# Kernel tuning notes

Hardware: AMD Instinct MI355X
Metric: run time of the kernel (lower is better)

The kernel has to match this reference:

```python
import jax, jax.numpy as jnp
import numpy as np

B, T, C, H = 8, 1024, 768, 12
HD = C // H  # 64, even for RoPE
ROPE_THETA = 10000.0


def precompute_freqs_cis(dim, end, theta=ROPE_THETA):
    # [end, dim//2, 2] with (cos, sin) in last axis
    freqs = 1.0 / theta ** (jnp.arange(0, dim // 2).astype(jnp.float32) / (dim // 2))
    t = jnp.arange(end)
    f = jnp.outer(t, freqs)
    return jnp.stack([jnp.cos(f), jnp.sin(f)], axis=-1)


def apply_rope(x, fc):
    # x: [B,T,H,hd]; fc: [T,1,hd//2,2] (broadcasts over B and H)
    xr = x.reshape(*x.shape[:-1], -1, 2)
    x_re, x_im = xr[..., 0], xr[..., 1]
    cos, sin = fc[..., 0], fc[..., 1]
    out_re = x_re * cos - x_im * sin
    out_im = x_re * sin + x_im * cos
    return jnp.stack([out_re, out_im], axis=-1).reshape(x.shape)


def setup_inputs() -> dict:
    key = jax.random.key(0)
    k0, k1, k2 = jax.random.split(key, 3)
    x = jax.random.normal(k0, (B, T, C), jnp.float32)
    Wqkv = jax.random.normal(k1, (C, 3 * C), jnp.float32) * 0.02
    bqkv = jnp.zeros((3 * C,), jnp.float32)
    Wproj = jax.random.normal(k2, (C, C), jnp.float32) * 0.02
    bproj = jnp.zeros((C,), jnp.float32)
    mask = jnp.tril(jnp.ones((T, T), jnp.int32))  # causal
    return {"x": x, "Wqkv": Wqkv, "bqkv": bqkv, "Wproj": Wproj, "bproj": bproj, "mask": mask}


def reference(x, Wqkv, bqkv, Wproj, bproj, mask):
    B_, T_, C_ = x.shape
    qkv = (x @ Wqkv + bqkv).reshape(B_, T_, 3, H, HD)
    q, k, v = qkv[:, :, 0], qkv[:, :, 1], qkv[:, :, 2]  # each [B,T,H,hd]
    fc = precompute_freqs_cis(HD, T_)[:, None]  # [T,1,hd//2,2]
    q = apply_rope(q, fc)
    k = apply_rope(k, fc)
    scale = 1.0 / jnp.sqrt(jnp.float32(HD))
    attn = jnp.einsum('bthd,bkhd->bhtk', q, k) * scale  # [B,H,T,T]
    neg = jnp.finfo(attn.dtype).min
    attn = jnp.where(mask[None, None, :, :] == 0, neg, attn)
    attn = jax.nn.softmax(attn, axis=-1)
    out = jnp.einsum('bhtk,bkhd->bthd', attn, v).reshape(B_, T_, C_)
    return out @ Wproj + bproj
```

## Files before the change

### kernel.cpp

```cpp
#include <hip/hip_runtime.h>
#include <cstdint>
#include <cstddef>

#define BB 8
#define TT 1024
#define CC 768
#define NH 12
#define HD 64

using bf16x8 = __attribute__((ext_vector_type(8))) short;
using f32x4  = __attribute__((ext_vector_type(4))) float;

static __device__ __forceinline__ short f2bf(float f) {
    uint32_t u;
    __builtin_memcpy(&u, &f, 4);
    u += 0x7FFFu + ((u >> 16) & 1u);
    return (short)(u >> 16);
}

static __device__ __forceinline__ uint32_t bfpack(float lo, float hi) {
    return (uint32_t)(uint16_t)f2bf(lo) | ((uint32_t)(uint16_t)f2bf(hi) << 16);
}

#define GLOAD_LDS16(gp, lp)                                                        \
    __builtin_amdgcn_global_load_lds(                                              \
        (const __attribute__((address_space(1))) void*)(gp),                       \
        (__attribute__((address_space(3))) void*)(lp), 16, 0, 0)

__global__ void fc_kernel(float2* __restrict__ fc) {
    int idx = blockIdx.x * 256 + threadIdx.x;
    int t = idx >> 5, p = idx & 31;
    float freq = powf(10000.0f, -(float)p / 32.0f);
    float a = (float)t * freq;
    fc[idx] = make_float2(cosf(a), sinf(a));
}

__global__ __launch_bounds__(256)
void cast_kernel(const float* __restrict__ in, short* __restrict__ out) {
    int i = (blockIdx.x * 256 + threadIdx.x) * 8;
    float4 f0 = *(const float4*)(in + i);
    float4 f1 = *(const float4*)(in + i + 4);
    bf16x8 h;
    h[0] = f2bf(f0.x); h[1] = f2bf(f0.y); h[2] = f2bf(f0.z); h[3] = f2bf(f0.w);
    h[4] = f2bf(f1.x); h[5] = f2bf(f1.y); h[6] = f2bf(f1.z); h[7] = f2bf(f1.w);
    *(bf16x8*)(out + i) = h;
}

__global__ __launch_bounds__(256)
void transpose_cast_kernel(const float* __restrict__ in, short* __restrict__ out,
                           int R, int Cdim) {
    __shared__ float tile[32][33];
    int tx = threadIdx.x, ty = threadIdx.y;
    int c0 = blockIdx.x * 32, r0 = blockIdx.y * 32;
#pragma unroll
    for (int i = 0; i < 4; i++)
        tile[ty + 8 * i][tx] = in[(size_t)(r0 + ty + 8 * i) * Cdim + c0 + tx];
    __syncthreads();
#pragma unroll
    for (int i = 0; i < 4; i++)
        out[(size_t)(c0 + ty + 8 * i) * R + r0 + tx] = f2bf(tile[tx][ty + 8 * i]);
}

__global__ __launch_bounds__(256)
void vtrans_kernel(const short* __restrict__ V, short* __restrict__ VT) {
    __shared__ short tl[64][72];
    const int tid = threadIdx.x;
    const int bh = blockIdx.y, t0 = blockIdx.x * 64;
    {
        int r = tid >> 2, cs = (tid & 3) * 16;
        const short* src = V + (size_t)bh * TT * HD + (size_t)(t0 + r) * HD + cs;
        *(bf16x8*)&tl[r][cs]     = *(const bf16x8*)src;
        *(bf16x8*)&tl[r][cs + 8] = *(const bf16x8*)(src + 8);
    }
    __syncthreads();
    {
        int d = tid >> 2, ts = (tid & 3) * 16;
        bf16x8 o0, o1;
#pragma unroll
        for (int e = 0; e < 8; e++) { o0[e] = tl[ts + e][d]; o1[e] = tl[ts + 8 + e][d]; }
        short* dst = VT + (size_t)bh * TT * HD + (size_t)d * TT + t0 + ts;
        *(bf16x8*)dst       = o0;
        *(bf16x8*)(dst + 8) = o1;
    }
}

template <int EPI>
__global__ __launch_bounds__(256)
void gemm_kernel(const short* __restrict__ Agl, const short* __restrict__ BT,
                 const float* __restrict__ bias,
                 short* __restrict__ Qb, short* __restrict__ Kb, short* __restrict__ Vb,
                 const float2* __restrict__ fc, float* __restrict__ out) {
    __shared__ __align__(16) char smem[49152];
    const int tid = threadIdx.x;
    const int lane = tid & 63, wid = tid >> 6;
    const int g = lane >> 4, c = lane & 15;
    const int wm = wid >> 1, wn = wid & 1;

    const int nx = gridDim.x;
    const int bid = blockIdx.y * nx + blockIdx.x;
    const int cpx = (nx * gridDim.y) >> 3;
    const int swz = (bid & 7) * cpx + (bid >> 3);
    const int m0 = (swz / nx) * 128, n0 = (swz % nx) * 128;

    const int sr = lane >> 2;
    const int scol = (((lane & 3) ^ ((sr >> 1) & 3)) << 3);
    const short* Abase = Agl + (size_t)(m0 + wid * 32 + sr) * 768 + scol;
    const short* Bbase = BT  + (size_t)(n0 + wid * 32 + sr) * 768 + scol;

#define STAGE(S, T, KH)                                                          \
    {                                                                            \
        size_t ko = (size_t)(T) * 64 + (KH) * 32;                                \
        GLOAD_LDS16(Abase + ko,            smem + (S) * 16384 + wid * 2048);     \
        GLOAD_LDS16(Abase + 16 * 768 + ko, smem + (S) * 16384 + wid * 2048 + 1024); \
        GLOAD_LDS16(Bbase + ko,            smem + (S) * 16384 + 8192 + wid * 2048); \
        GLOAD_LDS16(Bbase + 16 * 768 + ko, smem + (S) * 16384 + 8192 + wid * 2048 + 1024); \
    }

    const f32x4 zero4 = {0.f, 0.f, 0.f, 0.f};
    f32x4 acc[4][4];
#pragma unroll
    for (int i = 0; i < 4; i++)
#pragma unroll
        for (int j = 0; j < 4; j++) acc[i][j] = zero4;

    STAGE(0, 0, 0);
    STAGE(1, 0, 1);
    asm volatile("s_waitcnt vmcnt(4)" ::: "memory");
    asm volatile("s_barrier" ::: "memory");

    for (int t3 = 0; t3 < 12; t3 += 3) {
#pragma unroll
        for (int pp = 0; pp < 6; pp++) {
            const int slotR = pp % 3;
            const int slotS = (pp + 2) % 3;
            const int tile = t3 + (pp >> 1);
            const int kk = pp & 1;
            int tileS = tile + 1;
            if (tileS >= 12) tileS -= 12;

            const short* Ab = (const short*)(smem + slotR * 16384);
            const short* Bb = (const short*)(smem + slotR * 16384 + 8192);
            bf16x8 af[4], bfr[4];
#pragma unroll
            for (int mi = 0; mi < 4; mi++) {
                int row = wm * 64 + mi * 16 + c;
                af[mi] = *(const bf16x8*)&Ab[row * 32 + ((g ^ ((row >> 1) & 3)) << 3)];
            }
#pragma unroll
            for (int ni = 0; ni < 4; ni++) {
                int row = wn * 64 + ni * 16 + c;
                bfr[ni] = *(const bf16x8*)&Bb[row * 32 + ((g ^ ((row >> 1) & 3)) << 3)];
            }
            STAGE(slotS, tileS, kk);
            __builtin_amdgcn_s_setprio(1);
#pragma unroll
            for (int mi = 0; mi < 4; mi++)
#pragma unroll
                for (int ni = 0; ni < 4; ni++)
                    acc[mi][ni] = __builtin_amdgcn_mfma_f32_16x16x32_bf16(
                        af[mi], bfr[ni], acc[mi][ni], 0, 0, 0);
            __builtin_amdgcn_s_setprio(0);
            asm volatile("s_waitcnt vmcnt(4)" ::: "memory");
            asm volatile("s_barrier" ::: "memory");
        }
    }

    asm volatile("s_waitcnt vmcnt(0)" ::: "memory");
    asm volatile("s_barrier" ::: "memory");

    if (EPI == 0) {
        uint32_t* LD = (uint32_t*)smem;
#pragma unroll
        for (int ni = 0; ni < 4; ni++) {
            int nl = wn * 64 + ni * 16 + c;
            int n = n0 + nl;
            float bv = bias[n];
            int part = (n >= 1536) ? 2 : (n >= 768 ? 1 : 0);
            int d = (n - part * 768) & 63;
#pragma unroll
            for (int mi = 0; mi < 4; mi++) {
#pragma unroll
                for (int r = 0; r < 4; r++) {
                    int ml = wm * 64 + mi * 16 + g * 4 + r;
                    float v = acc[mi][ni][r] + bv;
                    float pv = __shfl_xor(v, 1);
                    if (!(c & 1)) {
                        float o0, o1;
                        if (part < 2) {
                            int t = (m0 + ml) & 1023;
                            float2 cs = fc[t * 32 + (d >> 1)];
                            o0 = v * cs.x - pv * cs.y;
                            o1 = v * cs.y + pv * cs.x;
                            if (part == 0) { o0 *= 0.125f; o1 *= 0.125f; }
                        } else { o0 = v; o1 = pv; }
                        LD[ml * 64 + ((nl >> 1) ^ (((ml >> 2) & 3) << 3))] = bfpack(o0, o1);
                    }
                }
            }
        }
        __syncthreads();
#pragma unroll
        for (int p = 0; p < 8; p++) {
            int ml = p * 16 + (tid >> 4);
            int wc = (tid & 15) * 4;
            int4 dat = *(const int4*)&LD[ml * 64 + (wc ^ (((ml >> 2) & 3) << 3))];
            int n = n0 + wc * 2;
            int part = (n >= 1536) ? 2 : (n >= 768 ? 1 : 0);
            int rem = n - part * 768;
            int h = rem >> 6, d = rem & 63;
            int m = m0 + ml, b = m >> 10, t = m & 1023;
            short* dst = (part == 0 ? Qb : part == 1 ? Kb : Vb)
                         + (((size_t)b * NH + h) * TT + t) * HD + d;
            *(int4*)dst = dat;
        }
    } else {
#pragma unroll
        for (int mi = 0; mi < 4; mi++)
#pragma unroll
            for (int ni = 0; ni < 4; ni++) {
                int n = n0 + wn * 64 + ni * 16 + c;
                float bv = bias[n];
#pragma unroll
                for (int r = 0; r < 4; r++) {
                    int m = m0 + wm * 64 + mi * 16 + g * 4 + r;
                    out[(size_t)m * CC + n] = acc[mi][ni][r] + bv;
                }
            }
    }
#undef STAGE
}

__global__ __launch_bounds__(256)
void attn_kernel(const short* __restrict__ Qb, const short* __restrict__ Kb,
                 const short* __restrict__ VT, short* __restrict__ Ob) {
    __shared__ uint32_t Pt[4][32][32];
    __shared__ uint32_t ot[128 * 32];
    const int tid = threadIdx.x, lane = tid & 63, wid = tid >> 6;
    const int g = lane >> 4, c = lane & 15;
    const int bh = blockIdx.x, qb = 7 - (int)blockIdx.y;
    const int b = bh / NH, h = bh % NH;
    const short* Qp = Qb + (size_t)bh * TT * HD;
    const short* Kp = Kb + (size_t)bh * TT * HD;
    const short* Vp = VT + (size_t)bh * TT * HD;
    const int q0 = qb * 128 + wid * 32;
    const int sw = (c & 7) << 2;

    bf16x8 qf[2][2];
#pragma unroll
    for (int qs = 0; qs < 2; qs++)
#pragma unroll
        for (int kh = 0; kh < 2; kh++)
            qf[qs][kh] = *(const bf16x8*)(Qp + (size_t)(q0 + qs * 16 + c) * HD + kh * 32 + g * 8);

    const f32x4 zero4 = {0.f, 0.f, 0.f, 0.f};
    f32x4 o[2][4];
#pragma unroll
    for (int qs = 0; qs < 2; qs++)
#pragma unroll
        for (int dt = 0; dt < 4; dt++) o[qs][dt] = zero4;
    float mrun[2] = {-1e30f, -1e30f}, lrun[2] = {0.f, 0.f};

    const int t0max = ((q0 + 31) >> 6) << 6;
    for (int t0 = 0; t0 <= t0max; t0 += 64) {
        f32x4 st[2][4];
#pragma unroll
        for (int nt = 0; nt < 4; nt++) {
            const short* kp = Kp + (size_t)(t0 + nt * 16 + c) * HD + g * 8;
            bf16x8 k0 = *(const bf16x8*)kp;
            bf16x8 k1 = *(const bf16x8*)(kp + 32);
#pragma unroll
            for (int qs = 0; qs < 2; qs++) {
                f32x4 z = zero4;
                z = __builtin_amdgcn_mfma_f32_16x16x32_bf16(k0, qf[qs][0], z, 0, 0, 0);
                z = __builtin_amdgcn_mfma_f32_16x16x32_bf16(k1, qf[qs][1], z, 0, 0, 0);
                st[qs][nt] = z;
            }
        }
        bf16x8 vf[2][4];
#pragma unroll
        for (int blk = 0; blk < 2; blk++)
#pragma unroll
            for (int dt = 0; dt < 4; dt++)
                vf[blk][dt] = *(const bf16x8*)(Vp + (size_t)(dt * 16 + c) * TT + t0 + blk * 32 + g * 8);
        if (t0 + 63 > q0) {
#pragma unroll
            for (int qs = 0; qs < 2; qs++) {
                int q = q0 + qs * 16 + c;
#pragma unroll
                for (int nt = 0; nt < 4; nt++)
#pragma unroll
                    for (int r = 0; r < 4; r++)
                        if (t0 + nt * 16 + g * 4 + r > q) st[qs][nt][r] = -1e30f;
            }
        }
#pragma unroll
        for (int qs = 0; qs < 2; qs++) {
            float mx = st[qs][0][0];
#pragma unroll
            for (int nt = 0; nt < 4; nt++)
#pragma unroll
                for (int r = 0; r < 4; r++) mx = fmaxf(mx, st[qs][nt][r]);
            mx = fmaxf(mx, __shfl_xor(mx, 16));
            mx = fmaxf(mx, __shfl_xor(mx, 32));
            float mnew = fmaxf(mrun[qs], mx);
            float al = __expf(mrun[qs] - mnew);
            mrun[qs] = mnew;
            float sm = 0.f;
#pragma unroll
            for (int nt = 0; nt < 4; nt++)
#pragma unroll
                for (int r = 0; r < 4; r++) {
                    float e = __expf(st[qs][nt][r] - mnew);
                    st[qs][nt][r] = e;
                    sm += e;
                }
            sm += __shfl_xor(sm, 16);
            sm += __shfl_xor(sm, 32);
            lrun[qs] = lrun[qs] * al + sm;
#pragma unroll
            for (int dt = 0; dt < 4; dt++) {
                o[qs][dt][0] *= al; o[qs][dt][1] *= al;
                o[qs][dt][2] *= al; o[qs][dt][3] *= al;
            }
            int row = qs * 16 + c;
#pragma unroll
            for (int nt = 0; nt < 4; nt++) {
                uint32_t w0 = bfpack(st[qs][nt][0], st[qs][nt][1]);
                uint32_t w1 = bfpack(st[qs][nt][2], st[qs][nt][3]);
                int wa = nt * 8 + 2 * g;
                Pt[wid][row][wa ^ sw]       = w0;
                Pt[wid][row][(wa + 1) ^ sw] = w1;
            }
        }
#pragma unroll
        for (int qs = 0; qs < 2; qs++) {
            int row = qs * 16 + c;
#pragma unroll
            for (int blk = 0; blk < 2; blk++) {
                bf16x8 pf = *(const bf16x8*)&Pt[wid][row][(blk * 16 + 4 * g) ^ sw];
#pragma unroll
                for (int dt = 0; dt < 4; dt++)
                    o[qs][dt] = __builtin_amdgcn_mfma_f32_16x16x32_bf16(
                        vf[blk][dt], pf, o[qs][dt], 0, 0, 0);
            }
        }
    }

#pragma unroll
    for (int qs = 0; qs < 2; qs++) {
        float inv = 1.0f / lrun[qs];
        int ql = wid * 32 + qs * 16 + c;
#pragma unroll
        for (int dt = 0; dt < 4; dt++) {
            uint32_t w0 = bfpack(o[qs][dt][0] * inv, o[qs][dt][1] * inv);
            uint32_t w1 = bfpack(o[qs][dt][2] * inv, o[qs][dt][3] * inv);
            int jc0 = dt * 8 + 2 * g;
            int jc1 = jc0 + 1;
            ot[ql * 32 + ((((jc0 >> 2) ^ (c & 7)) << 2) | (jc0 & 3))] = w0;
            ot[ql * 32 + ((((jc1 >> 2) ^ (c & 7)) << 2) | (jc1 & 3))] = w1;
        }
    }
    __syncthreads();
#pragma unroll
    for (int p = 0; p < 4; p++) {
        int q = (tid >> 3) + 32 * p;
        int jb = tid & 7;
        const uint32_t* src = &ot[q * 32 + ((jb ^ (q & 7)) << 2)];
        int4 w = *(const int4*)src;
        *(int4*)(Ob + ((size_t)b * TT + qb * 128 + q) * CC + h * HD + jb * 8) = w;
    }
}

extern "C" void kernel_launch(void* const* d_in, const int* in_sizes, int n_in,
                              void* d_out, int out_size, void* d_ws, size_t ws_size,
                              hipStream_t stream) {
    const float* x     = (const float*)d_in[0];
    const float* Wqkv  = (const float*)d_in[1];
    const float* bqkv  = (const float*)d_in[2];
    const float* Wproj = (const float*)d_in[3];
    const float* bproj = (const float*)d_in[4];

    char* ws = (char*)d_ws;
    short*  WqkvT  = (short*)(ws);
    short*  WprojT = (short*)(ws + 3538944);
    float2* fc     = (float2*)(ws + 3538944 + 1179648);
    short*  Qb     = (short*)(ws + 4980736);
    short*  Kb     = (short*)(ws + 4980736 + 1 * 12582912);
    short*  VOb    = (short*)(ws + 4980736 + 2 * 12582912);
    short*  VbT    = (short*)(ws + 4980736 + 3 * 12582912);
    short*  xb     = VbT;
    float*  out    = (float*)d_out;

    hipLaunchKernelGGL(fc_kernel, dim3(128), dim3(256), 0, stream, fc);
    hipLaunchKernelGGL(transpose_cast_kernel, dim3(72, 24), dim3(32, 8), 0, stream,
                       Wqkv, WqkvT, 768, 2304);
    hipLaunchKernelGGL(transpose_cast_kernel, dim3(24, 24), dim3(32, 8), 0, stream,
                       Wproj, WprojT, 768, 768);
    hipLaunchKernelGGL(cast_kernel, dim3(3072), dim3(256), 0, stream, x, xb);
    hipLaunchKernelGGL((gemm_kernel<0>), dim3(18, 64), dim3(256), 0, stream,
                       xb, WqkvT, bqkv, Qb, Kb, VOb, fc, (float*)nullptr);
    hipLaunchKernelGGL(vtrans_kernel, dim3(16, 96), dim3(256), 0, stream, VOb, VbT);
    hipLaunchKernelGGL(attn_kernel, dim3(96, 8), dim3(256), 0, stream, Qb, Kb, VbT, VOb);
    hipLaunchKernelGGL((gemm_kernel<1>), dim3(6, 64), dim3(256), 0, stream,
                       VOb, WprojT, bproj,
                       (short*)nullptr, (short*)nullptr, (short*)nullptr,
                       (const float2*)nullptr, out);
}
```

Before: 170.0 us.

## Enlarge GEMM tiles to 256x256 with 512 threads and four-stage LDS pipeline

Both GEMMs (QKV projection and output projection) move from 128x128 block tiles with 256 threads and a three-slot pipeline to 256x256 tiles with 512 threads (8 waves). The K loop now steps by 32 through a four-slot, 128 KB LDS ring, prefetching three tiles ahead. The QKV epilogue staging layout and its swizzle are widened to match. The aim is more operand reuse per byte loaded and fewer redundant global reads. In exchange the grids shrink to 288 and 96 blocks, which leaves CUs idle or adds tail waves on a 256-CU part, and the large LDS footprint limits occupancy.

```diff
diff --git a/kernel.cpp b/kernel.cpp
--- a/kernel.cpp
+++ b/kernel.cpp
@@ -85,82 +85,80 @@
 }
 
 template <int EPI>
-__global__ __launch_bounds__(256)
+__global__ __launch_bounds__(512, 2)
 void gemm_kernel(const short* __restrict__ Agl, const short* __restrict__ BT,
                  const float* __restrict__ bias,
                  short* __restrict__ Qb, short* __restrict__ Kb, short* __restrict__ Vb,
                  const float2* __restrict__ fc, float* __restrict__ out) {
-    __shared__ __align__(16) char smem[49152];
+    __shared__ __align__(16) char smem[131072];
     const int tid = threadIdx.x;
     const int lane = tid & 63, wid = tid >> 6;
     const int g = lane >> 4, c = lane & 15;
-    const int wm = wid >> 1, wn = wid & 1;
+    const int wm = wid >> 2, wn = wid & 3;
 
     const int nx = gridDim.x;
     const int bid = blockIdx.y * nx + blockIdx.x;
     const int cpx = (nx * gridDim.y) >> 3;
     const int swz = (bid & 7) * cpx + (bid >> 3);
-    const int m0 = (swz / nx) * 128, n0 = (swz % nx) * 128;
-
-    const int sr = lane >> 2;
-    const int scol = (((lane & 3) ^ ((sr >> 1) & 3)) << 3);
-    const short* Abase = Agl + (size_t)(m0 + wid * 32 + sr) * 768 + scol;
-    const short* Bbase = BT  + (size_t)(n0 + wid * 32 + sr) * 768 + scol;
-
-#define STAGE(S, T, KH)                                                          \
+    const int m0 = (swz / nx) * 256, n0 = (swz % nx) * 256;
+
+    const int srow = (lane >> 2);
+    const int schunk = (lane & 3) ^ ((lane >> 3) & 3);
+    const short* Ab0 = Agl + (size_t)(m0 + wid * 16 + srow) * 768 + schunk * 8;
+    const short* Bb0 = BT  + (size_t)(n0 + wid * 16 + srow) * 768 + schunk * 8;
+
+#define STAGE(S, T)                                                              \
     {                                                                            \
-        size_t ko = (size_t)(T) * 64 + (KH) * 32;                                \
-        GLOAD_LDS16(Abase + ko,            smem + (S) * 16384 + wid * 2048);     \
-        GLOAD_LDS16(Abase + 16 * 768 + ko, smem + (S) * 16384 + wid * 2048 + 1024); \
-        GLOAD_LDS16(Bbase + ko,            smem + (S) * 16384 + 8192 + wid * 2048); \
-        GLOAD_LDS16(Bbase + 16 * 768 + ko, smem + (S) * 16384 + 8192 + wid * 2048 + 1024); \
+        size_t ko = (size_t)(T) * 32;                                            \
+        GLOAD_LDS16(Ab0 + ko,             smem + (S) * 32768 + wid * 1024);      \
+        GLOAD_LDS16(Ab0 + 128 * 768 + ko, smem + (S) * 32768 + 8192 + wid * 1024); \
+        GLOAD_LDS16(Bb0 + ko,             smem + (S) * 32768 + 16384 + wid * 1024); \
+        GLOAD_LDS16(Bb0 + 128 * 768 + ko, smem + (S) * 32768 + 24576 + wid * 1024); \
     }
 
     const f32x4 zero4 = {0.f, 0.f, 0.f, 0.f};
-    f32x4 acc[4][4];
-#pragma unroll
-    for (int i = 0; i < 4; i++)
+    f32x4 acc[8][4];
+#pragma unroll
+    for (int i = 0; i < 8; i++)
 #pragma unroll
         for (int j = 0; j < 4; j++) acc[i][j] = zero4;
 
-    STAGE(0, 0, 0);
-    STAGE(1, 0, 1);
-    asm volatile("s_waitcnt vmcnt(4)" ::: "memory");
+    const int rchunk16 = (g ^ ((c >> 1) & 3)) << 4;
+
+    STAGE(0, 0);
+    STAGE(1, 1);
+    STAGE(2, 2);
+    asm volatile("s_waitcnt vmcnt(8)" ::: "memory");
     asm volatile("s_barrier" ::: "memory");
 
-    for (int t3 = 0; t3 < 12; t3 += 3) {
-#pragma unroll
-        for (int pp = 0; pp < 6; pp++) {
-            const int slotR = pp % 3;
-            const int slotS = (pp + 2) % 3;
-            const int tile = t3 + (pp >> 1);
-            const int kk = pp & 1;
-            int tileS = tile + 1;
-            if (tileS >= 12) tileS -= 12;
-
-            const short* Ab = (const short*)(smem + slotR * 16384);
-            const short* Bb = (const short*)(smem + slotR * 16384 + 8192);
-            bf16x8 af[4], bfr[4];
-#pragma unroll
-            for (int mi = 0; mi < 4; mi++) {
-                int row = wm * 64 + mi * 16 + c;
-                af[mi] = *(const bf16x8*)&Ab[row * 32 + ((g ^ ((row >> 1) & 3)) << 3)];
+    for (int w4 = 0; w4 < 24; w4 += 4) {
+#pragma unroll
+        for (int ww = 0; ww < 4; ww++) {
+            const int W = w4 + ww;
+            int tileS = W + 3;
+            if (tileS >= 24) tileS -= 24;
+            const char* slot = smem + ww * 32768;
+
+            bf16x8 af[8], bfr[4];
+#pragma unroll
+            for (int mi = 0; mi < 8; mi++) {
+                af[mi] = *(const bf16x8*)(slot + wm * 8192 + (mi * 16 + c) * 64 + rchunk16);
             }
 #pragma unroll
             for (int ni = 0; ni < 4; ni++) {
-                int row = wn * 64 + ni * 16 + c;
-                bfr[ni] = *(const bf16x8*)&Bb[row * 32 + ((g ^ ((row >> 1) & 3)) << 3)];
-            }
-            STAGE(slotS, tileS, kk);
+                bfr[ni] = *(const bf16x8*)(slot + 16384 + (wn >> 1) * 8192 +
+                                           ((wn & 1) * 64 + ni * 16 + c) * 64 + rchunk16);
+            }
+            STAGE((W + 3) & 3, tileS);
             __builtin_amdgcn_s_setprio(1);
 #pragma unroll
-            for (int mi = 0; mi < 4; mi++)
+            for (int mi = 0; mi < 8; mi++)
 #pragma unroll
                 for (int ni = 0; ni < 4; ni++)
                     acc[mi][ni] = __builtin_amdgcn_mfma_f32_16x16x32_bf16(
                         af[mi], bfr[ni], acc[mi][ni], 0, 0, 0);
             __builtin_amdgcn_s_setprio(0);
-            asm volatile("s_waitcnt vmcnt(4)" ::: "memory");
+            asm volatile("s_waitcnt vmcnt(8)" ::: "memory");
             asm volatile("s_barrier" ::: "memory");
         }
     }
@@ -178,10 +176,10 @@
             int part = (n >= 1536) ? 2 : (n >= 768 ? 1 : 0);
             int d = (n - part * 768) & 63;
 #pragma unroll
-            for (int mi = 0; mi < 4; mi++) {
+            for (int mi = 0; mi < 8; mi++) {
 #pragma unroll
                 for (int r = 0; r < 4; r++) {
-                    int ml = wm * 64 + mi * 16 + g * 4 + r;
+                    int ml = wm * 128 + mi * 16 + g * 4 + r;
                     float v = acc[mi][ni][r] + bv;
                     float pv = __shfl_xor(v, 1);
                     if (!(c & 1)) {
@@ -193,7 +191,7 @@
                             o1 = v * cs.y + pv * cs.x;
                             if (part == 0) { o0 *= 0.125f; o1 *= 0.125f; }
                         } else { o0 = v; o1 = pv; }
-                        LD[ml * 64 + ((nl >> 1) ^ (((ml >> 2) & 3) << 3))] = bfpack(o0, o1);
+                        LD[ml * 128 + ((nl >> 1) ^ ((ml & 7) << 2))] = bfpack(o0, o1);
                     }
                 }
             }
@@ -201,9 +199,11 @@
         __syncthreads();
 #pragma unroll
         for (int p = 0; p < 8; p++) {
-            int ml = p * 16 + (tid >> 4);
-            int wc = (tid & 15) * 4;
-            int4 dat = *(const int4*)&LD[ml * 64 + (wc ^ (((ml >> 2) & 3) << 3))];
+            int ml = p * 32 + (tid >> 4);
+            int sw = (ml & 7) << 2;
+            int wc = (tid & 15) * 8;
+            int4 d0 = *(const int4*)&LD[ml * 128 + (wc ^ sw)];
+            int4 d1 = *(const int4*)&LD[ml * 128 + ((wc + 4) ^ sw)];
             int n = n0 + wc * 2;
             int part = (n >= 1536) ? 2 : (n >= 768 ? 1 : 0);
             int rem = n - part * 768;
@@ -211,18 +211,19 @@
             int m = m0 + ml, b = m >> 10, t = m & 1023;
             short* dst = (part == 0 ? Qb : part == 1 ? Kb : Vb)
                          + (((size_t)b * NH + h) * TT + t) * HD + d;
-            *(int4*)dst = dat;
+            *(int4*)dst = d0;
+            *(int4*)(dst + 8) = d1;
         }
     } else {
 #pragma unroll
-        for (int mi = 0; mi < 4; mi++)
+        for (int mi = 0; mi < 8; mi++)
 #pragma unroll
             for (int ni = 0; ni < 4; ni++) {
                 int n = n0 + wn * 64 + ni * 16 + c;
                 float bv = bias[n];
 #pragma unroll
                 for (int r = 0; r < 4; r++) {
-                    int m = m0 + wm * 64 + mi * 16 + g * 4 + r;
+                    int m = m0 + wm * 128 + mi * 16 + g * 4 + r;
                     out[(size_t)m * CC + n] = acc[mi][ni][r] + bv;
                 }
             }
@@ -397,11 +398,11 @@
     hipLaunchKernelGGL(transpose_cast_kernel, dim3(24, 24), dim3(32, 8), 0, stream,
                        Wproj, WprojT, 768, 768);
     hipLaunchKernelGGL(cast_kernel, dim3(3072), dim3(256), 0, stream, x, xb);
-    hipLaunchKernelGGL((gemm_kernel<0>), dim3(18, 64), dim3(256), 0, stream,
+    hipLaunchKernelGGL((gemm_kernel<0>), dim3(9, 32), dim3(512), 0, stream,
                        xb, WqkvT, bqkv, Qb, Kb, VOb, fc, (float*)nullptr);
     hipLaunchKernelGGL(vtrans_kernel, dim3(16, 96), dim3(256), 0, stream, VOb, VbT);
     hipLaunchKernelGGL(attn_kernel, dim3(96, 8), dim3(256), 0, stream, Qb, Kb, VbT, VOb);
-    hipLaunchKernelGGL((gemm_kernel<1>), dim3(6, 64), dim3(256), 0, stream,
+    hipLaunchKernelGGL((gemm_kernel<1>), dim3(3, 32), dim3(512), 0, stream,
                        VOb, WprojT, bproj,
                        (short*)nullptr, (short*)nullptr, (short*)nullptr,
                        (const float2*)nullptr, out);
```

After: 193.3 us. 13.7% more time.
